# Kernel tuning notes

Measured on AMD Instinct MI355X. Metric: run time of the kernel, lower is better.

## Reference

```python
import jax, jax.numpy as jnp
import numpy as np

B, C, H, W = 16, 512, 32, 32
G = 8  # GroupNorm groups
EPS = 1e-5


def setup_inputs() -> dict:
    key = jax.random.key(0)
    ks = jax.random.split(key, 6)
    s = 1.0 / np.sqrt(C)
    return {
        "x": jax.random.normal(ks[0], (B, C, H, W), jnp.float32),
        "gamma": jnp.ones((C,), jnp.float32),
        "beta": jnp.zeros((C,), jnp.float32),
        "wq": jax.random.normal(ks[1], (C, C), jnp.float32) * s,
        "bq": jnp.zeros((C,), jnp.float32),
        "wk": jax.random.normal(ks[2], (C, C), jnp.float32) * s,
        "bk": jnp.zeros((C,), jnp.float32),
        "wv": jax.random.normal(ks[3], (C, C), jnp.float32) * s,
        "bv": jnp.zeros((C,), jnp.float32),
        "wp": jax.random.normal(ks[4], (C, C), jnp.float32) * s,
        "bp": jnp.zeros((C,), jnp.float32),
    }


def reference(x, gamma, beta, wq, bq, wk, bk, wv, bv, wp, bp):
    b, c, h, w = x.shape
    n = h * w
    # GroupNorm(8, C) over (C//G, H, W) per group
    xg = x.reshape(b, G, c // G, n)
    mean = xg.mean(axis=(2, 3), keepdims=True)
    var = xg.var(axis=(2, 3), keepdims=True)
    xn = ((xg - mean) * jax.lax.rsqrt(var + EPS)).reshape(b, c, n)
    xn = xn * gamma[:, None] + beta[:, None]
    # 1x1 conv projections: [C_out, C_in] @ [B, C_in, N]
    q = jnp.einsum('oc,bcn->bon', wq, xn) + bq[:, None]
    k = jnp.einsum('oc,bcn->bon', wk, xn) + bk[:, None]
    v = jnp.einsum('oc,bcn->bon', wv, xn) + bv[:, None]
    scale = 1.0 / (c ** 0.5)
    attn = jax.nn.softmax(jnp.einsum('bci,bcj->bij', q, k) * scale, axis=-1)
    # out[b,c,i] = sum_j v[b,c,j] * attn[b,i,j]
    out = jnp.einsum('bcj,bij->bci', v, attn)
    out = jnp.einsum('oc,bcn->bon', wp, out) + bp[:, None]
    return x + out.reshape(b, c, h, w)
```

## Files before the change

kernel.cpp:

```cpp
#include <hip/hip_runtime.h>

typedef __attribute__((ext_vector_type(8))) short short8;
typedef __attribute__((ext_vector_type(4))) short short4v;
typedef __attribute__((ext_vector_type(4))) float f32x4;
typedef __attribute__((ext_vector_type(4))) int i32x4;

__device__ __forceinline__ short f2bf(float f) {
  unsigned u = __builtin_bit_cast(unsigned, f);
  u = u + 0x7fffu + ((u >> 16) & 1u);
  return (short)(u >> 16);
}
__device__ __forceinline__ int q8(float v) {
  int q = (int)rintf(v * 16.f);
  return q < -127 ? -127 : (q > 127 ? 127 : q);
}

__device__ __forceinline__ int xcd_swz() {
  const int cpx = gridDim.x >> 3;
  return (blockIdx.x & 7) * cpx + (blockIdx.x >> 3);
}

__global__ __launch_bounds__(256) void pre_kernel(
    const float* __restrict__ x, float2* __restrict__ part,
    const float* __restrict__ wq, const float* __restrict__ wk,
    const float* __restrict__ wp, const float* __restrict__ wv,
    const float* __restrict__ bv, const float* __restrict__ bp,
    short* __restrict__ wp_bf, short* __restrict__ wvT,
    short* __restrict__ wqT, short* __restrict__ wkT,
    float* __restrict__ bias2, float* __restrict__ lsum,
    float* __restrict__ cadd) {
  const int blk = blockIdx.x, t = threadIdx.x;
  if (blk < 32) {
    const int w = t >> 6, lane = t & 63;
    const float4 b0 = *(const float4*)(bv + lane * 8);
    const float4 b1 = *(const float4*)(bv + lane * 8 + 4);
#pragma unroll
    for (int idx = 0; idx < 4; ++idx) {
      const int m = blk * 16 + w * 4 + idx;
      const float4 a0 = *(const float4*)(wp + (long)m * 512 + lane * 8);
      const float4 a1 = *(const float4*)(wp + (long)m * 512 + lane * 8 + 4);
      float s = a0.x * b0.x + a0.y * b0.y + a0.z * b0.z + a0.w * b0.w
              + a1.x * b1.x + a1.y * b1.y + a1.z * b1.z + a1.w * b1.w;
#pragma unroll
      for (int o = 32; o > 0; o >>= 1) s += __shfl_xor(s, o, 64);
      if (lane == 0) bias2[m] = bp[m] + s;
    }
  } else if (blk < 224) {
    const float* src; short* dst; int t2;
    if (blk < 96)       { t2 = blk - 32;  src = wv; dst = wvT; }
    else if (blk < 160) { t2 = blk - 96;  src = wq; dst = wqT; }
    else                { t2 = blk - 160; src = wk; dst = wkT; }
    const int tr = t2 >> 3, tc = t2 & 7;
    __shared__ float tile[64][65];
    const int r = t >> 2, q4 = t & 3;
    const float* s4 = src + (long)(tr * 64 + r) * 512 + tc * 64 + q4 * 16;
#pragma unroll
    for (int k = 0; k < 4; ++k) {
      float4 v = ((const float4*)s4)[k];
      tile[r][q4 * 16 + k * 4 + 0] = v.x;
      tile[r][q4 * 16 + k * 4 + 1] = v.y;
      tile[r][q4 * 16 + k * 4 + 2] = v.z;
      tile[r][q4 * 16 + k * 4 + 3] = v.w;
    }
    __syncthreads();
    const int oc = t >> 2, seg = t & 3;
    short tmp[16];
#pragma unroll
    for (int e = 0; e < 16; ++e) tmp[e] = f2bf(tile[seg * 16 + e][oc]);
    short* dp = dst + (long)(tc * 64 + oc) * 512 + tr * 64 + seg * 16;
    *(short8*)dp = *(short8*)&tmp[0];
    *(short8*)(dp + 8) = *(short8*)&tmp[8];
  } else if (blk < 228) {
    float4* p = (float4*)lsum;
    const int base = (blk - 224) * 1024 + t * 4;
#pragma unroll
    for (int k = 0; k < 4; ++k) p[base + k] = make_float4(0.f, 0.f, 0.f, 0.f);
  } else if (blk < 232) {
    float4* p = (float4*)cadd;
    const int base = (blk - 228) * 1024 + t * 4;
#pragma unroll
    for (int k = 0; k < 4; ++k) p[base + k] = make_float4(0.f, 0.f, 0.f, 0.f);
  } else if (blk < 488) {
    const int i4 = (blk - 232) * 1024 + t * 4;
    float4 v = *(const float4*)(wp + i4);
    short4v o;
    o.x = f2bf(v.x); o.y = f2bf(v.y); o.z = f2bf(v.z); o.w = f2bf(v.w);
    *(short4v*)(wp_bf + i4) = o;
  } else {
    const int blk2 = blk - 488;
    const float* base = x + (long)blk2 * 8192;
    float s = 0.f, ss = 0.f;
#pragma unroll
    for (int j = 0; j < 8; ++j) {
      float4 v = ((const float4*)base)[t + j * 256];
      s  += v.x + v.y + v.z + v.w;
      ss += v.x * v.x + v.y * v.y + v.z * v.z + v.w * v.w;
    }
    for (int o = 32; o > 0; o >>= 1) { s += __shfl_xor(s, o, 64); ss += __shfl_xor(ss, o, 64); }
    __shared__ float rs[4], rss[4];
    if ((t & 63) == 0) { rs[t >> 6] = s; rss[t >> 6] = ss; }
    __syncthreads();
    if (t == 0) {
      part[blk2] = make_float2(rs[0] + rs[1] + rs[2] + rs[3],
                               rss[0] + rss[1] + rss[2] + rss[3]);
    }
  }
}

#define BM 128
#define BK 64
enum { EPI_OUT = 5 };

__device__ __forceinline__ int swz_idx(int row, int k) {
  return row * 64 + ((((k >> 3) ^ row) & 7) << 3) + (k & 7);
}

__device__ __forceinline__ void gemm_core(
    const short* __restrict__ Ab, const short* __restrict__ Bb,
    short* lds, f32x4 (&acc)[4][4], int m0, int n0, int K, int tid) {
  const int lane = tid & 63, w = tid >> 6;
  const int wm = (w >> 1) * 64, wn = (w & 1) * 64;
  const int rowst = w * 32 + (lane >> 3);
  for (int k0 = 0; k0 < K; k0 += BK) {
    __syncthreads();
#pragma unroll
    for (int it = 0; it < 4; ++it) {
      int ci = w * 4 + it;
      int row = rowst + it * 8;
      int slot = (lane & 7) ^ (row & 7);
      const short* ga = Ab + (long)(m0 + row) * K + k0 + slot * 8;
      __builtin_amdgcn_global_load_lds(
          (const __attribute__((address_space(1))) void*)ga,
          (__attribute__((address_space(3))) void*)(lds + ci * 512), 16, 0, 0);
      const short* gb = Bb + (long)(n0 + row) * K + k0 + slot * 8;
      __builtin_amdgcn_global_load_lds(
          (const __attribute__((address_space(1))) void*)gb,
          (__attribute__((address_space(3))) void*)(lds + 8192 + ci * 512), 16, 0, 0);
    }
    __syncthreads();
#pragma unroll
    for (int kk = 0; kk < 2; ++kk) {
      short8 af[4], bf[4];
      const int kf = kk * 32 + (lane >> 4) * 8;
#pragma unroll
      for (int i = 0; i < 4; ++i) {
        af[i] = *(const short8*)(lds + swz_idx(wm + i * 16 + (lane & 15), kf));
        bf[i] = *(const short8*)(lds + 8192 + swz_idx(wn + i * 16 + (lane & 15), kf));
      }
#pragma unroll
      for (int i = 0; i < 4; ++i)
#pragma unroll
        for (int j = 0; j < 4; ++j)
          acc[i][j] = __builtin_amdgcn_mfma_f32_16x16x32_bf16(af[i], bf[j], acc[i][j], 0, 0, 0);
    }
  }
}

__global__ __launch_bounds__(256, 3) void wgemm_kernel(
    const short* __restrict__ wqT, const short* __restrict__ wkT,
    const short* __restrict__ wp_bf, const short* __restrict__ wvT,
    const float* __restrict__ bq, short* __restrict__ Wst,
    float* __restrict__ v1) {
  __shared__ short lds[2 * BM * BK];
  const int y = blockIdx.y, tid = threadIdx.x;
  if (y < 8) {
    const int which = y >> 2;
    const short* A  = which ? wp_bf : wqT;
    const short* Bt = which ? wvT   : wkT;
    const int m0 = (y & 3) * 128, n0 = blockIdx.x * 128;
    f32x4 acc[4][4] = {};
    gemm_core(A, Bt, lds, acc, m0, n0, 512, tid);
    const int lane = tid & 63, w = tid >> 6;
    const int wm = (w >> 1) * 64, wn = (w & 1) * 64;
    const int mb = m0 + wm + (lane >> 4) * 4;
    const int nb = n0 + wn + (lane & 15);
    short* C = Wst + which * 262144;
#pragma unroll
    for (int i = 0; i < 4; ++i)
#pragma unroll
      for (int r = 0; r < 4; ++r) {
        int m = mb + i * 16 + r;
#pragma unroll
        for (int j = 0; j < 4; ++j)
          C[(long)m * 512 + nb + j * 16] = f2bf(acc[i][j][r]);
      }
  } else {
    const int w = tid >> 6, lane = tid & 63;
    const int base_r = ((y - 8) * 4 + blockIdx.x) * 64;
    const float4 b0 = *(const float4*)(bq + lane * 8);
    const float4 b1 = *(const float4*)(bq + lane * 8 + 4);
#pragma unroll
    for (int idx = 0; idx < 16; ++idx) {
      const int c = base_r + w * 16 + idx;
      const short8 a = *(const short8*)(wkT + (long)c * 512 + lane * 8);
      float av[8];
#pragma unroll
      for (int e = 0; e < 8; ++e)
        av[e] = __builtin_bit_cast(float, ((unsigned)(unsigned short)a[e]) << 16);
      float s = av[0] * b0.x + av[1] * b0.y + av[2] * b0.z + av[3] * b0.w
              + av[4] * b1.x + av[5] * b1.y + av[6] * b1.z + av[7] * b1.w;
#pragma unroll
      for (int o = 32; o > 0; o >>= 1) s += __shfl_xor(s, o, 64);
      if (lane == 0) v1[c] = s;
    }
  }
}

#define TP 133
__global__ __launch_bounds__(256) void gn_norm_t(
    const float* __restrict__ x, const float2* __restrict__ part,
    const float* __restrict__ gamma, const float* __restrict__ beta,
    const float* __restrict__ v1, short* __restrict__ xnt,
    char* __restrict__ xi8, float* __restrict__ cadd) {
  const int blk = blockIdx.x;
  const int nc = blk & 7, g = (blk >> 3) & 7, b = blk >> 6;
  const int t = threadIdx.x;
  float s = 0.f, ss = 0.f;
#pragma unroll
  for (int j = 0; j < 8; ++j) {
    float2 p = part[(b * 8 + g) * 8 + j];
    s += p.x; ss += p.y;
  }
  const float mean = s * (1.f / 65536.f);
  const float var  = ss * (1.f / 65536.f) - mean * mean;
  const float rstd = rsqrtf(var + 1e-5f);

  const float* base = x + (long)(b * 512 + g * 64) * 1024 + nc * 128;
  __shared__ float tile[64][TP];
  const int row = t >> 2, c4 = t & 3;
#pragma unroll
  for (int j = 0; j < 8; ++j) {
    float4 v = *(const float4*)(base + (long)row * 1024 + (c4 + j * 4) * 4);
    *(float4*)&tile[row][(c4 + j * 4) * 4] = v;
  }
  const int cl4 = (t & 15) * 4;
  float ga[4], be[4];
#pragma unroll
  for (int j = 0; j < 4; ++j) {
    float gm = gamma[g * 64 + cl4 + j];
    ga[j] = gm * rstd;
    be[j] = beta[g * 64 + cl4 + j] - mean * ga[j];
  }
  const float4 v1c = *(const float4*)(v1 + g * 64 + cl4);
  __syncthreads();
  short* outb = xnt + (long)b * 524288 + (long)(nc * 128) * 512 + g * 64 + cl4;
  char* qb = xi8 + (long)b * 524288 + (long)(nc * 128) * 512 + g * 64 + cl4;
  float* cb = cadd + b * 1024 + nc * 128;
#pragma unroll
  for (int it = 0; it < 8; ++it) {
    const int tok = (t >> 4) + it * 16;
    float x0 = tile[cl4 + 0][tok] * ga[0] + be[0];
    float x1 = tile[cl4 + 1][tok] * ga[1] + be[1];
    float x2 = tile[cl4 + 2][tok] * ga[2] + be[2];
    float x3 = tile[cl4 + 3][tok] * ga[3] + be[3];
    short4v o;
    o.x = f2bf(x0); o.y = f2bf(x1); o.z = f2bf(x2); o.w = f2bf(x3);
    *(short4v*)(outb + (long)tok * 512) = o;
    unsigned pk = (q8(x0) & 255) | ((q8(x1) & 255) << 8)
                | ((q8(x2) & 255) << 16) | ((q8(x3) & 255) << 24);
    *(unsigned*)(qb + (long)tok * 512) = pk;
    float p = v1c.x * x0 + v1c.y * x1 + v1c.z * x2 + v1c.w * x3;
    p += __shfl_xor(p, 1, 64); p += __shfl_xor(p, 2, 64);
    p += __shfl_xor(p, 4, 64); p += __shfl_xor(p, 8, 64);
    if ((t & 15) == 0) atomicAdd(&cb[tok], p);
  }
}

__global__ __launch_bounds__(256, 3) void zu_gemm(
    const short* __restrict__ W, const short* __restrict__ xnt,
    char* __restrict__ zi, short* __restrict__ u) {
  __shared__ short lds[2 * BM * BK];
  const int lw = xcd_swz();
  const int b = lw >> 6, rem = lw & 63, y = rem >> 3, xg = rem & 7;
  const int which = y >> 2;
  const int m0 = y * BM;
  const int mloc0 = m0 - which * 512;
  const int n0 = xg * BM;
  const short* Bb = xnt + (long)b * 524288;
  const int tid = threadIdx.x, lane = tid & 63, w = tid >> 6;
  f32x4 acc[4][4] = {};
  gemm_core(W, Bb, lds, acc, m0, n0, 512, tid);

  const int wm = (w >> 1) * 64, wn = (w & 1) * 64;
  const int mb = mloc0 + wm + (lane >> 4) * 4;
  const int nb = n0 + wn + (lane & 15);
  if (which == 0) {
    char* C = zi + (long)b * 524288;
#pragma unroll
    for (int i = 0; i < 4; ++i) {
      int m = mb + i * 16;
#pragma unroll
      for (int j = 0; j < 4; ++j) {
        int n = nb + j * 16;
        unsigned pk = (q8(acc[i][j][0]) & 255) | ((q8(acc[i][j][1]) & 255) << 8)
                    | ((q8(acc[i][j][2]) & 255) << 16) | ((q8(acc[i][j][3]) & 255) << 24);
        *(unsigned*)(C + (long)n * 512 + m) = pk;
      }
    }
  } else {
    short* C = u + (long)b * 524288;
#pragma unroll
    for (int i = 0; i < 4; ++i) {
#pragma unroll
      for (int r = 0; r < 4; ++r) {
        int m = mb + i * 16 + r;
#pragma unroll
        for (int j = 0; j < 4; ++j) {
          int n = nb + j * 16;
          C[(long)m * 1024 + n] = f2bf(acc[i][j][r]);
        }
      }
    }
  }
}

__global__ __launch_bounds__(256, 3) void sexp_i8(
    const char* __restrict__ zi, const char* __restrict__ xi,
    short* __restrict__ S, float* __restrict__ lsum,
    const float* __restrict__ cadd, float scale) {
  __shared__ char lds[32768];
  const int lw = xcd_swz();
  const int b = lw >> 6, rem = lw & 63;
  const int m0 = (rem >> 3) * 128, n0 = (rem & 7) * 128;
  const char* Ab = zi + (long)b * 524288;
  const char* Bb = xi + (long)b * 524288;
  const int tid = threadIdx.x, lane = tid & 63, w = tid >> 6;
  const int wm = (w >> 1) * 64, wn = (w & 1) * 64;
  i32x4 acc[4][4] = {};

  long aoff[4], boff[4];
  int ldst[4];
#pragma unroll
  for (int it = 0; it < 4; ++it) {
    const int ci = w * 4 + it;
    const int row = ci * 8 + (lane >> 3);
    const int lg = (lane & 7) ^ (row & 7);
    aoff[it] = (long)(m0 + row) * 512 + lg * 16;
    boff[it] = (long)(n0 + row) * 512 + lg * 16;
    ldst[it] = ci * 1024 + lane * 16;
  }
  const int ar = lane & 15, g4 = lane >> 4;
  for (int k0 = 0; k0 < 512; k0 += 128) {
    __syncthreads();
#pragma unroll
    for (int it = 0; it < 4; ++it) {
      __builtin_amdgcn_global_load_lds(
          (const __attribute__((address_space(1))) void*)(Ab + aoff[it] + k0),
          (__attribute__((address_space(3))) void*)(lds + ldst[it]), 16, 0, 0);
      __builtin_amdgcn_global_load_lds(
          (const __attribute__((address_space(1))) void*)(Bb + boff[it] + k0),
          (__attribute__((address_space(3))) void*)(lds + 16384 + ldst[it]), 16, 0, 0);
    }
    __syncthreads();
#pragma unroll
    for (int kk = 0; kk < 2; ++kk) {
      i32x4 af[4], bf[4];
#pragma unroll
      for (int i = 0; i < 4; ++i) {
        const int rowA = wm + i * 16 + ar;
        af[i] = *(const i32x4*)(lds + rowA * 128 + (((kk * 4 + g4) ^ (rowA & 7)) * 16));
        const int rowB = wn + i * 16 + ar;
        bf[i] = *(const i32x4*)(lds + 16384 + rowB * 128 + (((kk * 4 + g4) ^ (rowB & 7)) * 16));
      }
#pragma unroll
      for (int i = 0; i < 4; ++i)
#pragma unroll
        for (int j = 0; j < 4; ++j)
          acc[i][j] = __builtin_amdgcn_mfma_i32_16x16x64_i8(af[i], bf[j], acc[i][j], 0, 0, 0);
    }
  }

  const int mb = m0 + wm + g4 * 4;
  const int nb = n0 + wn + ar;
  short* C = S + (long)b * 1048576;
  float4 ca[4];
#pragma unroll
  for (int i = 0; i < 4; ++i)
    ca[i] = *(const float4*)(cadd + b * 1024 + mb + i * 16);
  float rowsum[4] = {0.f, 0.f, 0.f, 0.f};
  const float qs = 1.f / 256.f;
#pragma unroll
  for (int j = 0; j < 4; ++j) {
    int n = nb + j * 16;
#pragma unroll
    for (int i = 0; i < 4; ++i) {
      int m = mb + i * 16;
      float e0 = __expf(((float)acc[i][j][0] * qs + ca[i].x) * scale);
      float e1 = __expf(((float)acc[i][j][1] * qs + ca[i].y) * scale);
      float e2 = __expf(((float)acc[i][j][2] * qs + ca[i].z) * scale);
      float e3 = __expf(((float)acc[i][j][3] * qs + ca[i].w) * scale);
      rowsum[j] += (e0 + e1) + (e2 + e3);
      short4v o;
      o.x = f2bf(e0); o.y = f2bf(e1); o.z = f2bf(e2); o.w = f2bf(e3);
      *(short4v*)(C + (long)n * 1024 + m) = o;
    }
  }
#pragma unroll
  for (int j = 0; j < 4; ++j) {
    rowsum[j] += __shfl_xor(rowsum[j], 16, 64);
    rowsum[j] += __shfl_xor(rowsum[j], 32, 64);
  }
  if (lane < 16) {
#pragma unroll
    for (int j = 0; j < 4; ++j)
      atomicAdd(&lsum[b * 1024 + nb + j * 16], rowsum[j]);
  }
}

template <int EPI>
__global__ __launch_bounds__(256, 3) void gemm_bt(
    const short* __restrict__ A, const short* __restrict__ Bt,
    void* __restrict__ Cv, const float* __restrict__ bias,
    const float* __restrict__ resid, float scale,
    int M, int N, int K, long aStr, long bStr, long cStr, long rStr,
    float* __restrict__ lsum, int bShift) {
  __shared__ short lds[2 * BM * BK];
  const int lw = xcd_swz();
  const int b = lw >> bShift, rem = lw & ((1 << bShift) - 1);
  const int m0 = (rem >> 3) * BM, n0 = (rem & 7) * BM;
  const short* Ab = A + (long)b * aStr;
  const short* Bb = Bt + (long)b * bStr;
  const int tid = threadIdx.x, lane = tid & 63, w = tid >> 6;
  f32x4 acc[4][4] = {};
  gemm_core(Ab, Bb, lds, acc, m0, n0, K, tid);

  const int wm = (w >> 1) * 64, wn = (w & 1) * 64;
  const int mb = m0 + wm + (lane >> 4) * 4;
  const int nb = n0 + wn + (lane & 15);
  float* C = (float*)Cv + (long)b * cStr;
  const float* R = resid + (long)b * rStr;
#pragma unroll
  for (int j = 0; j < 4; ++j) {
    int n = nb + j * 16;
    float rl = 1.0f / lsum[b * 1024 + n];
#pragma unroll
    for (int i = 0; i < 4; ++i) {
#pragma unroll
      for (int r = 0; r < 4; ++r) {
        int m = mb + i * 16 + r;
        C[(long)m * N + n] = acc[i][j][r] * rl + bias[m] + R[(long)m * N + n];
      }
    }
  }
}

extern "C" void kernel_launch(void* const* d_in, const int* in_sizes, int n_in,
                              void* d_out, int out_size, void* d_ws, size_t ws_size,
                              hipStream_t stream) {
  const float* x     = (const float*)d_in[0];
  const float* gamma = (const float*)d_in[1];
  const float* beta  = (const float*)d_in[2];
  const float* wq    = (const float*)d_in[3];
  const float* bq    = (const float*)d_in[4];
  const float* wk    = (const float*)d_in[5];
  const float* bk    = (const float*)d_in[6];
  const float* wv    = (const float*)d_in[7];
  const float* bv    = (const float*)d_in[8];
  const float* wp    = (const float*)d_in[9];
  const float* bp    = (const float*)d_in[10];
  (void)bk;

  char* ws = (char*)d_ws;
  short* Wst   = (short*)ws;
  float* bias2 = (float*)(ws + 1572864l);
  float* lsum  = (float*)(ws + 1638400l);
  float* v1    = (float*)(ws + 1703936l);
  float* cadd  = (float*)(ws + 1708032l);
  short* xnt   = (short*)(ws + 2097152l);
  char*  z_i8  = (char*)(ws + 18874368l);
  char*  x_i8  = (char*)(ws + 35651584l);
  short* u     = (short*)(ws + 52428800l);
  short* Sbf   = (short*)(ws + 69206016l);
  float2* gnpart = (float2*)Sbf;
  short* wp_bf = Sbf + 65536;
  short* wvT   = Sbf + 327680;
  short* wqT   = Sbf + 589824;
  short* wkT   = Sbf + 851968;

  pre_kernel<<<1512, 256, 0, stream>>>(
      x, gnpart, wq, wk, wp, wv, bv, bp, wp_bf, wvT, wqT, wkT,
      bias2, lsum, cadd);

  wgemm_kernel<<<dim3(4, 10), 256, 0, stream>>>(
      wqT, wkT, wp_bf, wvT, bq, Wst, v1);

  gn_norm_t<<<1024, 256, 0, stream>>>(
      x, gnpart, gamma, beta, v1, xnt, x_i8, cadd);

  zu_gemm<<<1024, 256, 0, stream>>>(Wst, xnt, z_i8, u);

  const float iscale = 0.044194173824159216f;
  sexp_i8<<<1024, 256, 0, stream>>>(z_i8, x_i8, Sbf, lsum, cadd, iscale);

  gemm_bt<EPI_OUT><<<512, 256, 0, stream>>>(
      u, Sbf, d_out, bias2, x, 1.f, 512, 1024, 1024,
      524288, 1048576, 524288, 524288, lsum, 5);
}
```

Measured before the change: 108.7 us.

## Store V-projection and softmax probabilities as FP8 and run output GEMM with FP8 MFMA

The u (value/projection) tensor and the exponentiated attention scores are now stored as FP8 instead of bf16, and the final output GEMM uses the fp8 MFMA instruction through a new fp8 core. This halves the bytes written by zu_gemm and sexp_i8 and read by the output GEMM, and uses a denser matrix instruction. The int8 GEMM loop in sexp_i8 is moved into a shared helper. The risk is larger quantization error, since exp values and u are stored with only a few mantissa bits.

Result: no change. 108.9 us (+0.2%).

```diff
diff --git a/kernel.cpp b/kernel.cpp
--- a/kernel.cpp
+++ b/kernel.cpp
@@ -109,7 +109,6 @@
 
 #define BM 128
 #define BK 64
-enum { EPI_OUT = 5 };
 
 __device__ __forceinline__ int swz_idx(int row, int k) {
   return row * 64 + ((((k >> 3) ^ row) & 7) << 3) + (k & 7);
@@ -152,6 +151,103 @@
 #pragma unroll
         for (int j = 0; j < 4; ++j)
           acc[i][j] = __builtin_amdgcn_mfma_f32_16x16x32_bf16(af[i], bf[j], acc[i][j], 0, 0, 0);
+    }
+  }
+}
+
+__device__ __forceinline__ void gemm_core_i8(
+    const char* __restrict__ Ab, const char* __restrict__ Bb,
+    char* lds, i32x4 (&acc)[4][4], int m0, int n0, int ldaB, int Kbytes, int tid) {
+  const int lane = tid & 63, w = tid >> 6;
+  const int wm = (w >> 1) * 64, wn = (w & 1) * 64;
+  long aoff[4], boff[4];
+  int ldst[4];
+#pragma unroll
+  for (int it = 0; it < 4; ++it) {
+    const int ci = w * 4 + it;
+    const int row = ci * 8 + (lane >> 3);
+    const int lg = (lane & 7) ^ (row & 7);
+    aoff[it] = (long)(m0 + row) * ldaB + lg * 16;
+    boff[it] = (long)(n0 + row) * ldaB + lg * 16;
+    ldst[it] = ci * 1024 + lane * 16;
+  }
+  const int ar = lane & 15, g4 = lane >> 4;
+  for (int k0 = 0; k0 < Kbytes; k0 += 128) {
+    __syncthreads();
+#pragma unroll
+    for (int it = 0; it < 4; ++it) {
+      __builtin_amdgcn_global_load_lds(
+          (const __attribute__((address_space(1))) void*)(Ab + aoff[it] + k0),
+          (__attribute__((address_space(3))) void*)(lds + ldst[it]), 16, 0, 0);
+      __builtin_amdgcn_global_load_lds(
+          (const __attribute__((address_space(1))) void*)(Bb + boff[it] + k0),
+          (__attribute__((address_space(3))) void*)(lds + 16384 + ldst[it]), 16, 0, 0);
+    }
+    __syncthreads();
+#pragma unroll
+    for (int kk = 0; kk < 2; ++kk) {
+      i32x4 af[4], bf[4];
+#pragma unroll
+      for (int i = 0; i < 4; ++i) {
+        const int rowA = wm + i * 16 + ar;
+        af[i] = *(const i32x4*)(lds + rowA * 128 + (((kk * 4 + g4) ^ (rowA & 7)) * 16));
+        const int rowB = wn + i * 16 + ar;
+        bf[i] = *(const i32x4*)(lds + 16384 + rowB * 128 + (((kk * 4 + g4) ^ (rowB & 7)) * 16));
+      }
+#pragma unroll
+      for (int i = 0; i < 4; ++i)
+#pragma unroll
+        for (int j = 0; j < 4; ++j)
+          acc[i][j] = __builtin_amdgcn_mfma_i32_16x16x64_i8(af[i], bf[j], acc[i][j], 0, 0, 0);
+    }
+  }
+}
+
+__device__ __forceinline__ void gemm_core_fp8(
+    const char* __restrict__ Ab, const char* __restrict__ Bb,
+    char* lds, f32x4 (&acc)[4][4], int m0, int n0, int ldaB, int Kbytes, int tid) {
+  const int lane = tid & 63, w = tid >> 6;
+  const int wm = (w >> 1) * 64, wn = (w & 1) * 64;
+  long aoff[4], boff[4];
+  int ldst[4];
+#pragma unroll
+  for (int it = 0; it < 4; ++it) {
+    const int ci = w * 4 + it;
+    const int row = ci * 8 + (lane >> 3);
+    const int lg = (lane & 7) ^ (row & 7);
+    aoff[it] = (long)(m0 + row) * ldaB + lg * 16;
+    boff[it] = (long)(n0 + row) * ldaB + lg * 16;
+    ldst[it] = ci * 1024 + lane * 16;
+  }
+  const int ar = lane & 15, g4 = lane >> 4;
+  const int gsel = g4 >> 1, hsel = (g4 & 1) * 8;
+  for (int k0 = 0; k0 < Kbytes; k0 += 128) {
+    __syncthreads();
+#pragma unroll
+    for (int it = 0; it < 4; ++it) {
+      __builtin_amdgcn_global_load_lds(
+          (const __attribute__((address_space(1))) void*)(Ab + aoff[it] + k0),
+          (__attribute__((address_space(3))) void*)(lds + ldst[it]), 16, 0, 0);
+      __builtin_amdgcn_global_load_lds(
+          (const __attribute__((address_space(1))) void*)(Bb + boff[it] + k0),
+          (__attribute__((address_space(3))) void*)(lds + 16384 + ldst[it]), 16, 0, 0);
+    }
+    __syncthreads();
+#pragma unroll
+    for (int c = 0; c < 4; ++c) {
+      long af[4], bf[4];
+#pragma unroll
+      for (int i = 0; i < 4; ++i) {
+        const int rowA = wm + i * 16 + ar;
+        af[i] = *(const long*)(lds + rowA * 128 + (((2 * c + gsel) ^ (rowA & 7)) * 16) + hsel);
+        const int rowB = wn + i * 16 + ar;
+        bf[i] = *(const long*)(lds + 16384 + rowB * 128 + (((2 * c + gsel) ^ (rowB & 7)) * 16) + hsel);
+      }
+#pragma unroll
+      for (int i = 0; i < 4; ++i)
+#pragma unroll
+        for (int j = 0; j < 4; ++j)
+          acc[i][j] = __builtin_amdgcn_mfma_f32_16x16x32_fp8_fp8(af[i], bf[j], acc[i][j], 0, 0, 0);
     }
   }
 }
@@ -268,7 +364,7 @@
 
 __global__ __launch_bounds__(256, 3) void zu_gemm(
     const short* __restrict__ W, const short* __restrict__ xnt,
-    char* __restrict__ zi, short* __restrict__ u) {
+    char* __restrict__ zi, char* __restrict__ u8) {
   __shared__ short lds[2 * BM * BK];
   const int lw = xcd_swz();
   const int b = lw >> 6, rem = lw & 63, y = rem >> 3, xg = rem & 7;
@@ -298,7 +394,7 @@
       }
     }
   } else {
-    short* C = u + (long)b * 524288;
+    char* C = u8 + (long)b * 524288;
 #pragma unroll
     for (int i = 0; i < 4; ++i) {
 #pragma unroll
@@ -307,7 +403,8 @@
 #pragma unroll
         for (int j = 0; j < 4; ++j) {
           int n = nb + j * 16;
-          C[(long)m * 1024 + n] = f2bf(acc[i][j][r]);
+          int pk = __builtin_amdgcn_cvt_pk_fp8_f32(acc[i][j][r], acc[i][j][r], 0, false);
+          C[(long)m * 1024 + n] = (char)(pk & 255);
         }
       }
     }
@@ -316,7 +413,7 @@
 
 __global__ __launch_bounds__(256, 3) void sexp_i8(
     const char* __restrict__ zi, const char* __restrict__ xi,
-    short* __restrict__ S, float* __restrict__ lsum,
+    char* __restrict__ P8, float* __restrict__ lsum,
     const float* __restrict__ cadd, float scale) {
   __shared__ char lds[32768];
   const int lw = xcd_swz();
@@ -327,52 +424,12 @@
   const int tid = threadIdx.x, lane = tid & 63, w = tid >> 6;
   const int wm = (w >> 1) * 64, wn = (w & 1) * 64;
   i32x4 acc[4][4] = {};
-
-  long aoff[4], boff[4];
-  int ldst[4];
-#pragma unroll
-  for (int it = 0; it < 4; ++it) {
-    const int ci = w * 4 + it;
-    const int row = ci * 8 + (lane >> 3);
-    const int lg = (lane & 7) ^ (row & 7);
-    aoff[it] = (long)(m0 + row) * 512 + lg * 16;
-    boff[it] = (long)(n0 + row) * 512 + lg * 16;
-    ldst[it] = ci * 1024 + lane * 16;
-  }
+  gemm_core_i8(Ab, Bb, lds, acc, m0, n0, 512, 512, tid);
+
   const int ar = lane & 15, g4 = lane >> 4;
-  for (int k0 = 0; k0 < 512; k0 += 128) {
-    __syncthreads();
-#pragma unroll
-    for (int it = 0; it < 4; ++it) {
-      __builtin_amdgcn_global_load_lds(
-          (const __attribute__((address_space(1))) void*)(Ab + aoff[it] + k0),
-          (__attribute__((address_space(3))) void*)(lds + ldst[it]), 16, 0, 0);
-      __builtin_amdgcn_global_load_lds(
-          (const __attribute__((address_space(1))) void*)(Bb + boff[it] + k0),
-          (__attribute__((address_space(3))) void*)(lds + 16384 + ldst[it]), 16, 0, 0);
-    }
-    __syncthreads();
-#pragma unroll
-    for (int kk = 0; kk < 2; ++kk) {
-      i32x4 af[4], bf[4];
-#pragma unroll
-      for (int i = 0; i < 4; ++i) {
-        const int rowA = wm + i * 16 + ar;
-        af[i] = *(const i32x4*)(lds + rowA * 128 + (((kk * 4 + g4) ^ (rowA & 7)) * 16));
-        const int rowB = wn + i * 16 + ar;
-        bf[i] = *(const i32x4*)(lds + 16384 + rowB * 128 + (((kk * 4 + g4) ^ (rowB & 7)) * 16));
-      }
-#pragma unroll
-      for (int i = 0; i < 4; ++i)
-#pragma unroll
-        for (int j = 0; j < 4; ++j)
-          acc[i][j] = __builtin_amdgcn_mfma_i32_16x16x64_i8(af[i], bf[j], acc[i][j], 0, 0, 0);
-    }
-  }
-
   const int mb = m0 + wm + g4 * 4;
   const int nb = n0 + wn + ar;
-  short* C = S + (long)b * 1048576;
+  char* C = P8 + (long)b * 1048576;
   float4 ca[4];
 #pragma unroll
   for (int i = 0; i < 4; ++i)
@@ -390,9 +447,9 @@
       float e2 = __expf(((float)acc[i][j][2] * qs + ca[i].z) * scale);
       float e3 = __expf(((float)acc[i][j][3] * qs + ca[i].w) * scale);
       rowsum[j] += (e0 + e1) + (e2 + e3);
-      short4v o;
-      o.x = f2bf(e0); o.y = f2bf(e1); o.z = f2bf(e2); o.w = f2bf(e3);
-      *(short4v*)(C + (long)n * 1024 + m) = o;
+      int pk = __builtin_amdgcn_cvt_pk_fp8_f32(e0, e1, 0, false);
+      pk = __builtin_amdgcn_cvt_pk_fp8_f32(e2, e3, pk, true);
+      *(unsigned*)(C + (long)n * 1024 + m) = (unsigned)pk;
     }
   }
 #pragma unroll
@@ -407,28 +464,26 @@
   }
 }
 
-template <int EPI>
-__global__ __launch_bounds__(256, 3) void gemm_bt(
-    const short* __restrict__ A, const short* __restrict__ Bt,
-    void* __restrict__ Cv, const float* __restrict__ bias,
-    const float* __restrict__ resid, float scale,
-    int M, int N, int K, long aStr, long bStr, long cStr, long rStr,
-    float* __restrict__ lsum, int bShift) {
-  __shared__ short lds[2 * BM * BK];
+__global__ __launch_bounds__(256, 3) void out_fp8(
+    const char* __restrict__ u8, const char* __restrict__ P8,
+    float* __restrict__ out, const float* __restrict__ bias2,
+    const float* __restrict__ x, const float* __restrict__ lsum) {
+  __shared__ char lds[32768];
   const int lw = xcd_swz();
-  const int b = lw >> bShift, rem = lw & ((1 << bShift) - 1);
-  const int m0 = (rem >> 3) * BM, n0 = (rem & 7) * BM;
-  const short* Ab = A + (long)b * aStr;
-  const short* Bb = Bt + (long)b * bStr;
+  const int b = lw >> 5, rem = lw & 31;
+  const int m0 = (rem >> 3) * 128, n0 = (rem & 7) * 128;
+  const char* Ab = u8 + (long)b * 524288;
+  const char* Bb = P8 + (long)b * 1048576;
   const int tid = threadIdx.x, lane = tid & 63, w = tid >> 6;
+  const int wm = (w >> 1) * 64, wn = (w & 1) * 64;
   f32x4 acc[4][4] = {};
-  gemm_core(Ab, Bb, lds, acc, m0, n0, K, tid);
-
-  const int wm = (w >> 1) * 64, wn = (w & 1) * 64;
-  const int mb = m0 + wm + (lane >> 4) * 4;
-  const int nb = n0 + wn + (lane & 15);
-  float* C = (float*)Cv + (long)b * cStr;
-  const float* R = resid + (long)b * rStr;
+  gemm_core_fp8(Ab, Bb, lds, acc, m0, n0, 1024, 1024, tid);
+
+  const int ar = lane & 15, g4 = lane >> 4;
+  const int mb = m0 + wm + g4 * 4;
+  const int nb = n0 + wn + ar;
+  float* C = out + (long)b * 524288;
+  const float* R = x + (long)b * 524288;
 #pragma unroll
   for (int j = 0; j < 4; ++j) {
     int n = nb + j * 16;
@@ -438,7 +493,7 @@
 #pragma unroll
       for (int r = 0; r < 4; ++r) {
         int m = mb + i * 16 + r;
-        C[(long)m * N + n] = acc[i][j][r] * rl + bias[m] + R[(long)m * N + n];
+        C[(long)m * 1024 + n] = acc[i][j][r] * rl + bias2[m] + R[(long)m * 1024 + n];
       }
     }
   }
@@ -469,13 +524,13 @@
   short* xnt   = (short*)(ws + 2097152l);
   char*  z_i8  = (char*)(ws + 18874368l);
   char*  x_i8  = (char*)(ws + 35651584l);
-  short* u     = (short*)(ws + 52428800l);
-  short* Sbf   = (short*)(ws + 69206016l);
-  float2* gnpart = (float2*)Sbf;
-  short* wp_bf = Sbf + 65536;
-  short* wvT   = Sbf + 327680;
-  short* wqT   = Sbf + 589824;
-  short* wkT   = Sbf + 851968;
+  char*  u_f8  = (char*)(ws + 52428800l);
+  char*  P8    = (char*)(ws + 69206016l);
+  float2* gnpart = (float2*)P8;
+  short* wp_bf = (short*)(P8 + 131072);
+  short* wvT   = (short*)(P8 + 655360);
+  short* wqT   = (short*)(P8 + 1179648);
+  short* wkT   = (short*)(P8 + 1703936);
 
   pre_kernel<<<1512, 256, 0, stream>>>(
       x, gnpart, wq, wk, wp, wv, bv, bp, wp_bf, wvT, wqT, wkT,
@@ -487,12 +542,10 @@
   gn_norm_t<<<1024, 256, 0, stream>>>(
       x, gnpart, gamma, beta, v1, xnt, x_i8, cadd);
 
-  zu_gemm<<<1024, 256, 0, stream>>>(Wst, xnt, z_i8, u);
+  zu_gemm<<<1024, 256, 0, stream>>>(Wst, xnt, z_i8, u_f8);
 
   const float iscale = 0.044194173824159216f;
-  sexp_i8<<<1024, 256, 0, stream>>>(z_i8, x_i8, Sbf, lsum, cadd, iscale);
-
-  gemm_bt<EPI_OUT><<<512, 256, 0, stream>>>(
-      u, Sbf, d_out, bias2, x, 1.f, 512, 1024, 1024,
-      524288, 1048576, 524288, 524288, lsum, 5);
-}
+  sexp_i8<<<1024, 256, 0, stream>>>(z_i8, x_i8, P8, lsum, cadd, iscale);
+
+  out_fp8<<<512, 256, 0, stream>>>(u_f8, P8, (float*)d_out, bias2, x, lsum);
+}
```
